# Performance work log

Hardware: AMD Instinct MI355X
Metric: run time of the kernel (lower is better)

Reference implementation:

```python
import jax, jax.numpy as jnp
import numpy as np
import math

E = 1024
H = 16
D = E // H  # 64
B, T, S = 4, 1024, 1024


def setup_inputs() -> dict:
    key = jax.random.key(0)
    ks = jax.random.split(key, 10)
    sd = 1.0 / math.sqrt(D)
    se = 1.0 / math.sqrt(E)
    return {
        "query": jax.random.normal(ks[0], (B, T, E), jnp.float32),
        "paragraph_encoding": jax.random.normal(ks[1], (S, E), jnp.float32),
        "Wq": jax.random.normal(ks[2], (D, D), jnp.float32) * sd,
        "bq": jax.random.normal(ks[3], (D,), jnp.float32) * sd,
        "Wk": jax.random.normal(ks[4], (D, D), jnp.float32) * sd,
        "bk": jax.random.normal(ks[5], (D,), jnp.float32) * sd,
        "Wv": jax.random.normal(ks[6], (D, D), jnp.float32) * sd,
        "bv": jax.random.normal(ks[7], (D,), jnp.float32) * sd,
        "Wout": jax.random.normal(ks[8], (E, E), jnp.float32) * se,
        "bout": jax.random.normal(ks[9], (E,), jnp.float32) * se,
    }


def reference(query, paragraph_encoding, Wq, bq, Wk, bk, Wv, bv, Wout, bout):
    b, t, _ = query.shape
    s = paragraph_encoding.shape[0]
    # [B, H, T, D]
    q = query.reshape(b, t, H, D).transpose(0, 2, 1, 3)
    # [H, S, D] -- key/value shared across batch
    p = paragraph_encoding.reshape(s, H, D).transpose(1, 0, 2)
    # per-head linear projections (torch Linear: x @ W.T + b)
    q = q @ Wq.T + bq
    k = p @ Wk.T + bk
    v = p @ Wv.T + bv
    # scores scaled by sqrt(embed_size), NOT head_dim (faithful to source)
    scores = jnp.einsum("bhtd,hsd->bhts", q, k) / math.sqrt(E)
    attn = jax.nn.softmax(scores, axis=-1)
    # (mask is None in this configuration; masking would occur AFTER softmax)
    context = jnp.einsum("bhts,hsd->bhtd", attn, v)
    context = context.transpose(0, 2, 1, 3).reshape(b, t, E)
    return context @ Wout.T + bout
```

## Files before the change

kernel.cpp:

```cpp
#include <hip/hip_runtime.h>


typedef __attribute__((ext_vector_type(8))) short short8v;
typedef __attribute__((ext_vector_type(4))) short short4v;
typedef __attribute__((ext_vector_type(4))) float float4v;

#define MFMA_BF16(A, B, C) __builtin_amdgcn_mfma_f32_16x16x32_bf16(A, B, C, 0, 0, 0)

#if __has_builtin(__builtin_amdgcn_exp2f)
#define EXP2F(x) __builtin_amdgcn_exp2f(x)
#else
#define EXP2F(x) exp2f(x)
#endif

#define QSCALE 0.045084220027780106f

__device__ __forceinline__ short f2bf(float f) {
  union { float f; unsigned u; } v; v.f = f;
  unsigned r = v.u + 0x7FFFu + ((v.u >> 16) & 1u);
  return (short)(r >> 16);
}

__global__ __launch_bounds__(256) void proj_qkv(
    const float* __restrict__ query, const float* __restrict__ para,
    const float* __restrict__ Wq, const float* __restrict__ bq,
    const float* __restrict__ Wk, const float* __restrict__ bk,
    const float* __restrict__ Wv, const float* __restrict__ bv,
    short* __restrict__ qs, short* __restrict__ kb, short* __restrict__ vt) {
  const int task = blockIdx.x * 4 + (threadIdx.x >> 6);
  const int lane = threadIdx.x & 63;
  const int g = lane >> 4, c = lane & 15;

  const float* W;
  const float* bias;
  const float* xrow;
  int type, h, tile, bh = 0;
  if (task < 4096) {
    type = 0; bh = task >> 6; tile = task & 63; h = bh & 15;
    xrow = query + ((bh >> 4) * 1024 + tile * 16 + c) * 1024 + h * 64;
    W = Wq; bias = bq;
  } else if (task < 5120) {
    int idx = task - 4096;
    type = 1; h = idx >> 6; tile = idx & 63;
    xrow = para + (tile * 16 + c) * 1024 + h * 64;
    W = Wk; bias = bk;
  } else {
    int idx = task - 5120;
    type = 2; h = idx >> 6; tile = idx & 63;
    xrow = para + (tile * 16 + c) * 1024 + h * 64;
    W = Wv; bias = bv;
  }

  short8v af[2];
#pragma unroll
  for (int kh = 0; kh < 2; ++kh) {
    const float* xp = xrow + kh * 32 + g * 8;
    float4v x0 = *(const float4v*)xp;
    float4v x1 = *(const float4v*)(xp + 4);
    af[kh] = (short8v){ f2bf(x0.x), f2bf(x0.y), f2bf(x0.z), f2bf(x0.w),
                        f2bf(x1.x), f2bf(x1.y), f2bf(x1.z), f2bf(x1.w) };
  }

#pragma unroll
  for (int dn = 0; dn < 4; ++dn) {
    float4v acc = (float4v){0.f, 0.f, 0.f, 0.f};
#pragma unroll
    for (int kh = 0; kh < 2; ++kh) {
      const float* wp = W + (dn * 16 + c) * 64 + kh * 32 + g * 8;
      float4v w0 = *(const float4v*)wp;
      float4v w1 = *(const float4v*)(wp + 4);
      short8v bfr = (short8v){ f2bf(w0.x), f2bf(w0.y), f2bf(w0.z), f2bf(w0.w),
                               f2bf(w1.x), f2bf(w1.y), f2bf(w1.z), f2bf(w1.w) };
      acc = MFMA_BF16(af[kh], bfr, acc);
    }
    const float bc = bias[dn * 16 + c];
    if (type == 0) {
#pragma unroll
      for (int r = 0; r < 4; ++r) {
        const int t = tile * 16 + 4 * g + r;
        qs[(bh * 1024 + t) * 64 + dn * 16 + c] = f2bf((acc[r] + bc) * QSCALE);
      }
    } else if (type == 1) {
#pragma unroll
      for (int r = 0; r < 4; ++r) {
        const int s = tile * 16 + 4 * g + r;
        kb[(h * 1024 + s) * 64 + dn * 16 + c] = f2bf(acc[r] + bc);
      }
    } else {
      short4v pk = (short4v){ f2bf(acc[0] + bc), f2bf(acc[1] + bc),
                              f2bf(acc[2] + bc), f2bf(acc[3] + bc) };
      *(short4v*)(vt + (h * 64 + dn * 16 + c) * 1024 + tile * 16 + 4 * g) = pk;
    }
  }
}

__global__ __launch_bounds__(256) void cvt_wout(const float* __restrict__ wsrc,
                                                short* __restrict__ wdst) {
  const int i = (blockIdx.x * 256 + threadIdx.x) * 8;
  float4v x0 = *(const float4v*)(wsrc + i);
  float4v x1 = *(const float4v*)(wsrc + i + 4);
  short8v v = (short8v){ f2bf(x0.x), f2bf(x0.y), f2bf(x0.z), f2bf(x0.w),
                         f2bf(x1.x), f2bf(x1.y), f2bf(x1.z), f2bf(x1.w) };
  *(short8v*)(wdst + i) = v;
}

__global__ __launch_bounds__(256, 4) void attn_fwd(
    const short* __restrict__ qs, const short* __restrict__ kb,
    const short* __restrict__ vt, short* __restrict__ ctx) {
  __shared__ __align__(16) short kv[2][4096];
  __shared__ __align__(16) short plds[4][2][16][40];
  const int tid = threadIdx.x;
  const int w = tid >> 6;
  const int lane = tid & 63;
  const int g = lane >> 4, c = lane & 15;
  const int bh = blockIdx.x & 63;
  const int b = bh >> 4, h = bh & 15;
  const int t0 = (blockIdx.x >> 6) * 128 + w * 32;

  const int kr = tid >> 3, kq = (tid & 7) ^ (kr & 7);
  const char* ksrc = (const char*)(kb + h * 65536) + kr * 128 + kq * 16;
  const int vd = tid >> 2, vq = (tid & 3) ^ ((vd >> 1) & 3);
  const char* vsrc = (const char*)(vt + h * 65536) + vd * 2048 + vq * 16;
  char* kdst = (char*)&kv[0][0] + tid * 16;
  char* vdst = (char*)&kv[0][0] + 4096 + tid * 16;

  int koff[2][2];
#pragma unroll
  for (int sm = 0; sm < 2; ++sm)
#pragma unroll
    for (int kh = 0; kh < 2; ++kh)
      koff[sm][kh] = (sm * 16 + c) * 128 + (((kh * 4 + g) ^ (c & 7)) * 16);
  int voff[4];
#pragma unroll
  for (int nt = 0; nt < 4; ++nt)
    voff[nt] = 4096 + (nt * 16 + c) * 64 + ((g ^ ((c >> 1) & 3)) * 16);

  const short* qbase = qs + (bh * 1024 + t0) * 64;
  short8v qf[2][2];
#pragma unroll
  for (int tn = 0; tn < 2; ++tn)
#pragma unroll
    for (int kh = 0; kh < 2; ++kh)
      qf[tn][kh] = *(const short8v*)(qbase + (tn * 16 + c) * 64 + kh * 32 + g * 8);

  float4v cacc[2][4];
#pragma unroll
  for (int tn = 0; tn < 2; ++tn)
#pragma unroll
    for (int nt = 0; nt < 4; ++nt)
      cacc[tn][nt] = (float4v){0.f, 0.f, 0.f, 0.f};
  float4v dacc[2];
  dacc[0] = (float4v){0.f, 0.f, 0.f, 0.f};
  dacc[1] = (float4v){0.f, 0.f, 0.f, 0.f};
  const short obf = (short)0x3F80;
  const short8v ones = (short8v){obf, obf, obf, obf, obf, obf, obf, obf};

  short8v sk = *(const short8v*)ksrc;
  short8v sv = *(const short8v*)vsrc;
  *(short8v*)kdst = sk;
  *(short8v*)vdst = sv;

  const char* kv0 = (const char*)&kv[0][0];
  for (int i = 0; i < 32; ++i) {
    __syncthreads();
    if (i < 31) {
      sk = *(const short8v*)(ksrc + (i + 1) * 4096);
      sv = *(const short8v*)(vsrc + (i + 1) * 64);
    }

    const char* kvb = kv0 + (i & 1) * 8192;
    short8v kf[2][2];
#pragma unroll
    for (int sm = 0; sm < 2; ++sm)
#pragma unroll
      for (int kh = 0; kh < 2; ++kh)
        kf[sm][kh] = *(const short8v*)(kvb + koff[sm][kh]);
    short8v vf[4];
#pragma unroll
    for (int nt = 0; nt < 4; ++nt)
      vf[nt] = *(const short8v*)(kvb + voff[nt]);

#pragma unroll
    for (int sm = 0; sm < 2; ++sm)
#pragma unroll
      for (int tn = 0; tn < 2; ++tn) {
        float4v z = (float4v){0.f, 0.f, 0.f, 0.f};
        z = MFMA_BF16(kf[sm][0], qf[tn][0], z);
        z = MFMA_BF16(kf[sm][1], qf[tn][1], z);
        const float p0 = EXP2F(z[0]);
        const float p1 = EXP2F(z[1]);
        const float p2 = EXP2F(z[2]);
        const float p3 = EXP2F(z[3]);
        short4v pk = (short4v){ f2bf(p0), f2bf(p1), f2bf(p2), f2bf(p3) };
        *(short4v*)&plds[w][tn][c][sm * 16 + 4 * g] = pk;
      }

    asm volatile("" ::: "memory");

    short8v pa[2];
#pragma unroll
    for (int tn = 0; tn < 2; ++tn)
      pa[tn] = *(const short8v*)&plds[w][tn][c][g * 8];

#pragma unroll
    for (int tn = 0; tn < 2; ++tn) {
#pragma unroll
      for (int nt = 0; nt < 4; ++nt)
        cacc[tn][nt] = MFMA_BF16(pa[tn], vf[nt], cacc[tn][nt]);
      dacc[tn] = MFMA_BF16(pa[tn], ones, dacc[tn]);
    }

    asm volatile("" ::: "memory");

    if (i < 31) {
      *(short8v*)(kdst + ((i + 1) & 1) * 8192) = sk;
      *(short8v*)(vdst + ((i + 1) & 1) * 8192) = sv;
    }
  }

  const int orow0 = b * 1024 + t0;
#pragma unroll
  for (int tn = 0; tn < 2; ++tn) {
    float inv[4];
#pragma unroll
    for (int r = 0; r < 4; ++r) inv[r] = 1.0f / dacc[tn][r];
#pragma unroll
    for (int nt = 0; nt < 4; ++nt)
#pragma unroll
      for (int r = 0; r < 4; ++r) {
        const int row = orow0 + tn * 16 + 4 * g + r;
        ctx[row * 1024 + h * 64 + nt * 16 + c] = f2bf(cacc[tn][nt][r] * inv[r]);
      }
  }
}

__global__ __launch_bounds__(512, 4) void out_proj(
    const short* __restrict__ ctx, const short* __restrict__ wb,
    const float* __restrict__ bout, float* __restrict__ out) {
  __shared__ __align__(16) short ab[2][6144];
  const int w = threadIdx.x >> 6;
  const int lane = threadIdx.x & 63;
  const int g = lane >> 4, c = lane & 15;
  const int mblk = (blockIdx.x & 31) * 128;
  const int n0 = (blockIdx.x >> 5) * 64;

  const int srow = w * 16 + (lane >> 2);
  const int sq = (lane & 3) ^ ((lane >> 3) & 3);
  const char* asrc = (const char*)ctx + (mblk + srow) * 2048 + sq * 16;
  char* adst = (char*)&ab[0][0] + w * 1024 + lane * 16;
  const char* bsrc = (const char*)wb + (n0 + srow) * 2048 + sq * 16;
  char* bdst = (char*)&ab[0][0] + 8192 + w * 1024 + lane * 16;

  const int sw = (g ^ ((c >> 1) & 3)) * 16;
  const int aoff = (w * 16 + c) * 64 + sw;
  int boff[4];
#pragma unroll
  for (int nt = 0; nt < 4; ++nt)
    boff[nt] = 8192 + (nt * 16 + c) * 64 + sw;

  float4v acc[4];
#pragma unroll
  for (int nt = 0; nt < 4; ++nt) acc[nt] = (float4v){0.f, 0.f, 0.f, 0.f};

  short8v sa = *(const short8v*)asrc;
  short8v sb = (short8v){0, 0, 0, 0, 0, 0, 0, 0};
  if (w < 4) sb = *(const short8v*)bsrc;
  *(short8v*)adst = sa;
  if (w < 4) *(short8v*)bdst = sb;

  const char* ab0 = (const char*)&ab[0][0];
  for (int i = 0; i < 32; ++i) {
    __syncthreads();
    if (i < 31) {
      sa = *(const short8v*)(asrc + (i + 1) * 64);
      if (w < 4) sb = *(const short8v*)(bsrc + (i + 1) * 64);
    }
    const char* abb = ab0 + (i & 1) * 12288;
    short8v a = *(const short8v*)(abb + aoff);
    short8v bb[4];
#pragma unroll
    for (int nt = 0; nt < 4; ++nt)
      bb[nt] = *(const short8v*)(abb + boff[nt]);
#pragma unroll
    for (int nt = 0; nt < 4; ++nt)
      acc[nt] = MFMA_BF16(a, bb[nt], acc[nt]);
    if (i < 31) {
      *(short8v*)(adst + ((i + 1) & 1) * 12288) = sa;
      if (w < 4) *(short8v*)(bdst + ((i + 1) & 1) * 12288) = sb;
    }
  }

  float bs[4];
#pragma unroll
  for (int nt = 0; nt < 4; ++nt) bs[nt] = bout[n0 + nt * 16 + c];

  const int m0 = mblk + w * 16;
#pragma unroll
  for (int nt = 0; nt < 4; ++nt)
#pragma unroll
    for (int r = 0; r < 4; ++r)
      out[(m0 + 4 * g + r) * 1024 + n0 + nt * 16 + c] = acc[nt][r] + bs[nt];
}

extern "C" void kernel_launch(void* const* d_in, const int* in_sizes, int n_in,
                              void* d_out, int out_size, void* d_ws, size_t ws_size,
                              hipStream_t stream) {
  const float* query = (const float*)d_in[0];
  const float* para  = (const float*)d_in[1];
  const float* Wq = (const float*)d_in[2];
  const float* bq = (const float*)d_in[3];
  const float* Wk = (const float*)d_in[4];
  const float* bk = (const float*)d_in[5];
  const float* Wv = (const float*)d_in[6];
  const float* bv = (const float*)d_in[7];
  const float* Wout = (const float*)d_in[8];
  const float* bout = (const float*)d_in[9];
  float* out = (float*)d_out;

  char* ws = (char*)d_ws;
  short* qs  = (short*)(ws);
  short* kb  = (short*)(ws + (8u  << 20));
  short* vt  = (short*)(ws + (10u << 20));
  short* ctx = (short*)(ws + (12u << 20));
  short* wb  = (short*)(ws + (20u << 20));

  proj_qkv<<<dim3(1536), dim3(256), 0, stream>>>(query, para, Wq, bq, Wk, bk,
                                                 Wv, bv, qs, kb, vt);
  cvt_wout<<<dim3(512), dim3(256), 0, stream>>>(Wout, wb);
  attn_fwd<<<dim3(512), dim3(256), 0, stream>>>(qs, kb, vt, ctx);
  out_proj<<<dim3(512), dim3(512), 0, stream>>>(ctx, wb, bout, out);
}
```

Before: 71.19 us.

## Fuse Wout conversion into projection kernel, retile out_proj, add MFMA priority hints

The Wout fp32-to-bf16 conversion moves into the QKV projection kernel as extra tasks, which removes one kernel launch. out_proj is retiled so each wave computes a 32x32 output tile, loading A fragments straight from global memory into registers. Only the B tile is staged through a smaller LDS buffer, which cuts LDS traffic and footprint. s_setprio hints are wrapped around the MFMA blocks in the attention and out_proj loops, with the risk that uncoalesced direct A loads from global memory add latency.

```diff
diff --git a/kernel.cpp b/kernel.cpp
--- a/kernel.cpp
+++ b/kernel.cpp
@@ -26,10 +26,28 @@
     const float* __restrict__ Wq, const float* __restrict__ bq,
     const float* __restrict__ Wk, const float* __restrict__ bk,
     const float* __restrict__ Wv, const float* __restrict__ bv,
-    short* __restrict__ qs, short* __restrict__ kb, short* __restrict__ vt) {
+    const float* __restrict__ Wout,
+    short* __restrict__ qs, short* __restrict__ kb, short* __restrict__ vt,
+    short* __restrict__ wb) {
   const int task = blockIdx.x * 4 + (threadIdx.x >> 6);
   const int lane = threadIdx.x & 63;
   const int g = lane >> 4, c = lane & 15;
+
+  if (task >= 6144) {
+    const int j = task - 6144;
+    const float* src = Wout + j * 2048;
+    short* dst = wb + j * 2048;
+#pragma unroll
+    for (int it = 0; it < 4; ++it) {
+      const int off = it * 512 + lane * 8;
+      float4v x0 = *(const float4v*)(src + off);
+      float4v x1 = *(const float4v*)(src + off + 4);
+      short8v v = (short8v){ f2bf(x0.x), f2bf(x0.y), f2bf(x0.z), f2bf(x0.w),
+                             f2bf(x1.x), f2bf(x1.y), f2bf(x1.z), f2bf(x1.w) };
+      *(short8v*)(dst + off) = v;
+    }
+    return;
+  }
 
   const float* W;
   const float* bias;
@@ -94,16 +112,6 @@
   }
 }
 
-__global__ __launch_bounds__(256) void cvt_wout(const float* __restrict__ wsrc,
-                                                short* __restrict__ wdst) {
-  const int i = (blockIdx.x * 256 + threadIdx.x) * 8;
-  float4v x0 = *(const float4v*)(wsrc + i);
-  float4v x1 = *(const float4v*)(wsrc + i + 4);
-  short8v v = (short8v){ f2bf(x0.x), f2bf(x0.y), f2bf(x0.z), f2bf(x0.w),
-                         f2bf(x1.x), f2bf(x1.y), f2bf(x1.z), f2bf(x1.w) };
-  *(short8v*)(wdst + i) = v;
-}
-
 __global__ __launch_bounds__(256, 4) void attn_fwd(
     const short* __restrict__ qs, const short* __restrict__ kb,
     const short* __restrict__ vt, short* __restrict__ ctx) {
@@ -185,8 +193,10 @@
 #pragma unroll
       for (int tn = 0; tn < 2; ++tn) {
         float4v z = (float4v){0.f, 0.f, 0.f, 0.f};
+        __builtin_amdgcn_s_setprio(1);
         z = MFMA_BF16(kf[sm][0], qf[tn][0], z);
         z = MFMA_BF16(kf[sm][1], qf[tn][1], z);
+        __builtin_amdgcn_s_setprio(0);
         const float p0 = EXP2F(z[0]);
         const float p1 = EXP2F(z[1]);
         const float p2 = EXP2F(z[2]);
@@ -202,6 +212,7 @@
     for (int tn = 0; tn < 2; ++tn)
       pa[tn] = *(const short8v*)&plds[w][tn][c][g * 8];
 
+    __builtin_amdgcn_s_setprio(1);
 #pragma unroll
     for (int tn = 0; tn < 2; ++tn) {
 #pragma unroll
@@ -209,6 +220,7 @@
         cacc[tn][nt] = MFMA_BF16(pa[tn], vf[nt], cacc[tn][nt]);
       dacc[tn] = MFMA_BF16(pa[tn], ones, dacc[tn]);
     }
+    __builtin_amdgcn_s_setprio(0);
 
     asm volatile("" ::: "memory");
 
@@ -237,69 +249,81 @@
 __global__ __launch_bounds__(512, 4) void out_proj(
     const short* __restrict__ ctx, const short* __restrict__ wb,
     const float* __restrict__ bout, float* __restrict__ out) {
-  __shared__ __align__(16) short ab[2][6144];
+  __shared__ __align__(16) short bl[2][2048];
   const int w = threadIdx.x >> 6;
   const int lane = threadIdx.x & 63;
   const int g = lane >> 4, c = lane & 15;
+  const int wm = w >> 1, wn = w & 1;
   const int mblk = (blockIdx.x & 31) * 128;
   const int n0 = (blockIdx.x >> 5) * 64;
 
   const int srow = w * 16 + (lane >> 2);
   const int sq = (lane & 3) ^ ((lane >> 3) & 3);
-  const char* asrc = (const char*)ctx + (mblk + srow) * 2048 + sq * 16;
-  char* adst = (char*)&ab[0][0] + w * 1024 + lane * 16;
   const char* bsrc = (const char*)wb + (n0 + srow) * 2048 + sq * 16;
-  char* bdst = (char*)&ab[0][0] + 8192 + w * 1024 + lane * 16;
+  char* bdst = (char*)&bl[0][0] + w * 1024 + lane * 16;
 
   const int sw = (g ^ ((c >> 1) & 3)) * 16;
-  const int aoff = (w * 16 + c) * 64 + sw;
-  int boff[4];
-#pragma unroll
-  for (int nt = 0; nt < 4; ++nt)
-    boff[nt] = 8192 + (nt * 16 + c) * 64 + sw;
-
-  float4v acc[4];
-#pragma unroll
-  for (int nt = 0; nt < 4; ++nt) acc[nt] = (float4v){0.f, 0.f, 0.f, 0.f};
-
-  short8v sa = *(const short8v*)asrc;
+  int boff[2];
+#pragma unroll
+  for (int nt = 0; nt < 2; ++nt)
+    boff[nt] = (wn * 32 + nt * 16 + c) * 64 + sw;
+
+  const short* abase[2];
+#pragma unroll
+  for (int mt = 0; mt < 2; ++mt)
+    abase[mt] = ctx + (mblk + wm * 32 + mt * 16 + c) * 1024 + g * 8;
+
+  float4v acc[2][2];
+#pragma unroll
+  for (int mt = 0; mt < 2; ++mt)
+#pragma unroll
+    for (int nt = 0; nt < 2; ++nt)
+      acc[mt][nt] = (float4v){0.f, 0.f, 0.f, 0.f};
+
   short8v sb = (short8v){0, 0, 0, 0, 0, 0, 0, 0};
-  if (w < 4) sb = *(const short8v*)bsrc;
-  *(short8v*)adst = sa;
-  if (w < 4) *(short8v*)bdst = sb;
-
-  const char* ab0 = (const char*)&ab[0][0];
+  if (w < 4) { sb = *(const short8v*)bsrc; *(short8v*)bdst = sb; }
+  short8v a[2];
+  a[0] = *(const short8v*)abase[0];
+  a[1] = *(const short8v*)abase[1];
+
+  const char* bl0 = (const char*)&bl[0][0];
   for (int i = 0; i < 32; ++i) {
     __syncthreads();
+    short8v an[2];
     if (i < 31) {
-      sa = *(const short8v*)(asrc + (i + 1) * 64);
       if (w < 4) sb = *(const short8v*)(bsrc + (i + 1) * 64);
-    }
-    const char* abb = ab0 + (i & 1) * 12288;
-    short8v a = *(const short8v*)(abb + aoff);
-    short8v bb[4];
-#pragma unroll
-    for (int nt = 0; nt < 4; ++nt)
-      bb[nt] = *(const short8v*)(abb + boff[nt]);
-#pragma unroll
-    for (int nt = 0; nt < 4; ++nt)
-      acc[nt] = MFMA_BF16(a, bb[nt], acc[nt]);
+      an[0] = *(const short8v*)(abase[0] + (i + 1) * 32);
+      an[1] = *(const short8v*)(abase[1] + (i + 1) * 32);
+    }
+    const char* bb = bl0 + (i & 1) * 4096;
+    short8v bf0 = *(const short8v*)(bb + boff[0]);
+    short8v bf1 = *(const short8v*)(bb + boff[1]);
+    __builtin_amdgcn_s_setprio(1);
+    acc[0][0] = MFMA_BF16(a[0], bf0, acc[0][0]);
+    acc[0][1] = MFMA_BF16(a[0], bf1, acc[0][1]);
+    acc[1][0] = MFMA_BF16(a[1], bf0, acc[1][0]);
+    acc[1][1] = MFMA_BF16(a[1], bf1, acc[1][1]);
+    __builtin_amdgcn_s_setprio(0);
     if (i < 31) {
-      *(short8v*)(adst + ((i + 1) & 1) * 12288) = sa;
-      if (w < 4) *(short8v*)(bdst + ((i + 1) & 1) * 12288) = sb;
-    }
-  }
-
-  float bs[4];
-#pragma unroll
-  for (int nt = 0; nt < 4; ++nt) bs[nt] = bout[n0 + nt * 16 + c];
-
-  const int m0 = mblk + w * 16;
-#pragma unroll
-  for (int nt = 0; nt < 4; ++nt)
-#pragma unroll
-    for (int r = 0; r < 4; ++r)
-      out[(m0 + 4 * g + r) * 1024 + n0 + nt * 16 + c] = acc[nt][r] + bs[nt];
+      if (w < 4) *(short8v*)(bdst + ((i + 1) & 1) * 4096) = sb;
+      a[0] = an[0];
+      a[1] = an[1];
+    }
+  }
+
+  float bs[2];
+#pragma unroll
+  for (int nt = 0; nt < 2; ++nt) bs[nt] = bout[n0 + wn * 32 + nt * 16 + c];
+
+  const int m0 = mblk + wm * 32;
+#pragma unroll
+  for (int mt = 0; mt < 2; ++mt)
+#pragma unroll
+    for (int nt = 0; nt < 2; ++nt)
+#pragma unroll
+      for (int r = 0; r < 4; ++r)
+        out[(m0 + mt * 16 + 4 * g + r) * 1024 + n0 + wn * 32 + nt * 16 + c] =
+            acc[mt][nt][r] + bs[nt];
 }
 
 extern "C" void kernel_launch(void* const* d_in, const int* in_sizes, int n_in,
@@ -324,9 +348,8 @@
   short* ctx = (short*)(ws + (12u << 20));
   short* wb  = (short*)(ws + (20u << 20));
 
-  proj_qkv<<<dim3(1536), dim3(256), 0, stream>>>(query, para, Wq, bq, Wk, bk,
-                                                 Wv, bv, qs, kb, vt);
-  cvt_wout<<<dim3(512), dim3(256), 0, stream>>>(Wout, wb);
+  proj_qkv<<<dim3(1664), dim3(256), 0, stream>>>(query, para, Wq, bq, Wk, bk,
+                                                 Wv, bv, Wout, qs, kb, vt, wb);
   attn_fwd<<<dim3(512), dim3(256), 0, stream>>>(qs, kb, vt, ctx);
   out_proj<<<dim3(512), dim3(512), 0, stream>>>(ctx, wb, bout, out);
 }
```

Result: slower. 83.90 us (+17.9%).
